# Optimization experiments

Hardware: AMD Instinct MI355X
Metric: run time of the kernel (lower is better)

The kernel has to match this reference:

```python
import jax, jax.numpy as jnp
import numpy as np

B, T_ENC, H, L, OUT, S_DEC = 32, 512, 512, 2, 128, 128
KV = 2 * H  # bidirectional encoder output width


def setup_inputs() -> dict:
    key = jax.random.key(0)
    ks = jax.random.split(key, 17)
    s = 0.05  # keep recurrent dynamics stable
    return {
        "encoder_output": jax.random.normal(ks[0], (B, T_ENC, KV), jnp.float32),
        "h0": jax.random.normal(ks[1], (L, B, H), jnp.float32) * s,
        "c0": jax.random.normal(ks[2], (L, B, H), jnp.float32) * s,
        "Wk": jax.random.normal(ks[3], (KV, KV), jnp.float32) * s,
        "Wq": jax.random.normal(ks[4], (KV, H), jnp.float32) * s,
        "Wv": jax.random.normal(ks[5], (KV, KV), jnp.float32) * s,
        "We": jax.random.normal(ks[6], (1, KV), jnp.float32) * s,
        "wih0": jax.random.normal(ks[7], (4 * H, OUT + KV), jnp.float32) * s,
        "whh0": jax.random.normal(ks[8], (4 * H, H), jnp.float32) * s,
        "bih0": jax.random.normal(ks[9], (4 * H,), jnp.float32) * s,
        "bhh0": jax.random.normal(ks[10], (4 * H,), jnp.float32) * s,
        "wih1": jax.random.normal(ks[11], (4 * H, H), jnp.float32) * s,
        "whh1": jax.random.normal(ks[12], (4 * H, H), jnp.float32) * s,
        "bih1": jax.random.normal(ks[13], (4 * H,), jnp.float32) * s,
        "bhh1": jax.random.normal(ks[14], (4 * H,), jnp.float32) * s,
        "fc_w": jax.random.normal(ks[15], (OUT, H), jnp.float32) * s,
        "fc_b": jax.random.normal(ks[16], (OUT,), jnp.float32) * s,
        "seq_length": S_DEC,
    }


def _lstm_cell(x, h, c, wih, whh, bih, bhh):
    # torch gate order: i, f, g, o
    g = x @ wih.T + h @ whh.T + bih + bhh
    i, f, gg, o = jnp.split(g, 4, axis=-1)
    c_new = jax.nn.sigmoid(f) * c + jax.nn.sigmoid(i) * jnp.tanh(gg)
    h_new = jax.nn.sigmoid(o) * jnp.tanh(c_new)
    return h_new, c_new


def reference(encoder_output, h0, c0, Wk, Wq, Wv, We, wih0, whh0, bih0, bhh0,
              wih1, whh1, bih1, bhh1, fc_w, fc_b, seq_length):
    # precomputed projections (key_layer / value_layer, no bias)
    key = encoder_output @ Wk.T      # [B, T_enc, KV]
    value = encoder_output @ Wv.T    # [B, T_enc, KV]

    def step(carry, _):
        h, c, y = carry  # h,c: [L,B,H]; y: [B,OUT]
        # Bahdanau attention, query = layer-0 hidden state
        q = h[0] @ Wq.T                                         # [B, KV]
        scores = jnp.einsum('btk,k->bt', jnp.tanh(q[:, None, :] + key), We[0])
        alpha = jax.nn.softmax(scores, axis=-1)                 # [B, T_enc]
        context = jnp.einsum('bt,btd->bd', alpha, value)        # [B, KV]
        x = jnp.concatenate([y, context], axis=-1)              # [B, OUT+KV]
        h0n, c0n = _lstm_cell(x, h[0], c[0], wih0, whh0, bih0, bhh0)
        h1n, c1n = _lstm_cell(h0n, h[1], c[1], wih1, whh1, bih1, bhh1)
        y_hat = jax.nn.relu(h1n @ fc_w.T + fc_b)                # [B, OUT]
        new_carry = (jnp.stack([h0n, h1n]), jnp.stack([c0n, c1n]), 1.0 + y_hat)
        return new_carry, y_hat

    y_init = jnp.zeros((h0.shape[1], fc_b.shape[0]), jnp.float32)  # SOS = 0.0
    _, ys = jax.lax.scan(step, (h0, c0, y_init), None, length=seq_length)
    return jnp.transpose(ys, (1, 0, 2))  # [B, seq_length, OUT]
```

## Files before the change

kernel.cpp:

```cpp
#include <hip/hip_runtime.h>
#include <hip/hip_bf16.h>
#include <cstdint>

#define TE    512
#define SD    128

typedef unsigned short u16;
typedef u16 u16x4 __attribute__((ext_vector_type(4)));
typedef u16 u16x8 __attribute__((ext_vector_type(8)));

#define QO    0
#define SCO   32768
#define CTXO  81920
#define YO    114688
#define H0O   118784
#define C0O   151552
#define H1O   184320
#define C1O   217088
#define ST_N  249856

__device__ __forceinline__ float b2f(u16 v) { return __uint_as_float(((unsigned)v) << 16); }
__device__ __forceinline__ u16 f2b(float f) {
  unsigned u = __float_as_uint(f);
  return (u16)((u + 0x7FFFu + ((u >> 16) & 1u)) >> 16);
}
__device__ __forceinline__ float tanh_f(float x) {
  float xc = fminf(12.f, fmaxf(-12.f, x));
  float e  = __expf(2.f * xc);
  return __fdividef(e - 1.f, e + 1.f);
}
__device__ __forceinline__ float sigm(float x) {
  float xc = fminf(30.f, fmaxf(-30.f, x));
  return __fdividef(1.f, 1.f + __expf(-xc));
}

__global__ __launch_bounds__(256)
void gemm_kv(const float* __restrict__ E, const float* __restrict__ Wk,
             const float* __restrict__ Wv, u16* __restrict__ key, u16* __restrict__ value) {
  const float* B = blockIdx.z ? Wv : Wk;
  u16* outp = blockIdx.z ? value : key;
  __shared__ float Asm[16][68], Bsm[16][68];
  const int tid = threadIdx.x;
  const int tm = blockIdx.x * 64, tn = blockIdx.y * 64;
  const int lr = tid >> 2, lc = (tid & 3) * 4;
  const int tx = tid & 15, ty = tid >> 4;
  float acc[4][4] = {};
  for (int k0 = 0; k0 < 1024; k0 += 16) {
    float4 av = *(const float4*)(&E[(long)(tm + lr) * 1024 + k0 + lc]);
    float4 bv = *(const float4*)(&B[(long)(tn + lr) * 1024 + k0 + lc]);
    Asm[lc][lr] = av.x; Asm[lc + 1][lr] = av.y; Asm[lc + 2][lr] = av.z; Asm[lc + 3][lr] = av.w;
    Bsm[lc][lr] = bv.x; Bsm[lc + 1][lr] = bv.y; Bsm[lc + 2][lr] = bv.z; Bsm[lc + 3][lr] = bv.w;
    __syncthreads();
#pragma unroll
    for (int kk = 0; kk < 16; ++kk) {
      float4 a4 = *(const float4*)(&Asm[kk][ty * 4]);
      float4 b4 = *(const float4*)(&Bsm[kk][tx * 4]);
      acc[0][0] += a4.x * b4.x; acc[0][1] += a4.x * b4.y; acc[0][2] += a4.x * b4.z; acc[0][3] += a4.x * b4.w;
      acc[1][0] += a4.y * b4.x; acc[1][1] += a4.y * b4.y; acc[1][2] += a4.y * b4.z; acc[1][3] += a4.y * b4.w;
      acc[2][0] += a4.z * b4.x; acc[2][1] += a4.z * b4.y; acc[2][2] += a4.z * b4.z; acc[2][3] += a4.z * b4.w;
      acc[3][0] += a4.w * b4.x; acc[3][1] += a4.w * b4.y; acc[3][2] += a4.w * b4.z; acc[3][3] += a4.w * b4.w;
    }
    __syncthreads();
  }
#pragma unroll
  for (int i = 0; i < 4; ++i)
#pragma unroll
    for (int j = 0; j < 4; ++j)
      outp[(long)(tm + ty * 4 + i) * 1024 + tn + tx * 4 + j] = f2b(acc[i][j]);
}

__global__ __launch_bounds__(256)
void init_state(const float* __restrict__ h0, const float* __restrict__ c0, float* __restrict__ st) {
  int i = blockIdx.x * 256 + threadIdx.x;
  st[H0O + i] = h0[i];
  st[H1O + i] = h0[16384 + i];
  st[C0O + i] = c0[i];
  st[C1O + i] = c0[16384 + i];
  if (i < 4096) st[YO + i] = 0.f;
}

__global__ __launch_bounds__(256)
void qproj(const float* __restrict__ h0, const float* __restrict__ Wq, float* __restrict__ st) {
  __shared__ float hr[512];
  const int b = blockIdx.x >> 2, o = (blockIdx.x & 3) * 256 + threadIdx.x;
  for (int i = threadIdx.x; i < 512; i += 256) hr[i] = h0[b * 512 + i];
  __syncthreads();
  float acc = 0.f;
  for (int k = 0; k < 512; k += 4) {
    float4 wv = *(const float4*)(&Wq[(long)o * 512 + k]);
    acc += hr[k] * wv.x + hr[k + 1] * wv.y + hr[k + 2] * wv.z + hr[k + 3] * wv.w;
  }
  st[QO + b * 1024 + o] = acc;
}

__global__ __launch_bounds__(256)
void stepA(const u16* __restrict__ key, const float* __restrict__ We, float* __restrict__ st) {
  const int tid = threadIdx.x, wv = tid >> 6, ln = tid & 63;
  const int b = blockIdx.x >> 4, tc = blockIdx.x & 15, t0 = tc * 32;
  float qr[16], wer[16];
  {
    const float* qp = st + QO + b * 1024 + ln * 16;
#pragma unroll
    for (int j = 0; j < 16; ++j) qr[j] = qp[j];
#pragma unroll
    for (int j = 0; j < 16; j += 4) {
      float4 w4 = *(const float4*)(&We[ln * 16 + j]);
      wer[j] = w4.x; wer[j + 1] = w4.y; wer[j + 2] = w4.z; wer[j + 3] = w4.w;
    }
  }
  const u16* kbase = key + ((long)(b * TE + t0) << 10) + ln * 16;
#pragma unroll
  for (int u = 0; u < 4; ++u) {
    const int tt0 = wv + u * 8, tt1 = wv + u * 8 + 4;
    const u16* kr0 = kbase + ((long)tt0 << 10);
    const u16* kr1 = kbase + ((long)tt1 << 10);
    u16x8 a0 = *(const u16x8*)kr0, a1 = *(const u16x8*)(kr0 + 8);
    u16x8 b0 = *(const u16x8*)kr1, b1 = *(const u16x8*)(kr1 + 8);
    float p0 = 0.f, p1 = 0.f;
#pragma unroll
    for (int j = 0; j < 8; ++j) {
      p0 += tanh_f(qr[j] + b2f(a0[j])) * wer[j];
      p1 += tanh_f(qr[j] + b2f(b0[j])) * wer[j];
    }
#pragma unroll
    for (int j = 0; j < 8; ++j) {
      p0 += tanh_f(qr[8 + j] + b2f(a1[j])) * wer[8 + j];
      p1 += tanh_f(qr[8 + j] + b2f(b1[j])) * wer[8 + j];
    }
    for (int off = 32; off; off >>= 1) {
      p0 += __shfl_down(p0, off);
      p1 += __shfl_down(p1, off);
    }
    if (ln == 0) {
      st[SCO + b * 512 + t0 + tt0] = p0;
      st[SCO + b * 512 + t0 + tt1] = p1;
    }
  }
}

__global__ __launch_bounds__(256)
void stepB(const u16* __restrict__ value, const float* __restrict__ fcw,
           const float* __restrict__ fcb, float* __restrict__ st,
           float* __restrict__ out, int s) {
  __shared__ float sm[1576];
  const int tid = threadIdx.x, wv = tid >> 6, ln = tid & 63;
  if (blockIdx.x < 256) {
    const int b = blockIdx.x >> 3, dc = blockIdx.x & 7;
    float* al = sm; float* rr = sm + 512; float* gp = sm + 520;
    al[tid]       = st[SCO + b * 512 + tid];
    al[tid + 256] = st[SCO + b * 512 + tid + 256];
    __syncthreads();
    float m = fmaxf(al[tid], al[tid + 256]);
    for (int off = 32; off; off >>= 1) m = fmaxf(m, __shfl_xor(m, off));
    if (ln == 0) rr[wv] = m;
    __syncthreads();
    const float M = fmaxf(fmaxf(rr[0], rr[1]), fmaxf(rr[2], rr[3]));
    float e0 = __expf(al[tid] - M), e1 = __expf(al[tid + 256] - M);
    float l = e0 + e1;
    for (int off = 32; off; off >>= 1) l += __shfl_xor(l, off);
    if (ln == 0) rr[4 + wv] = l;
    __syncthreads();
    const float inv = __fdividef(1.f, rr[4] + rr[5] + rr[6] + rr[7]);
    al[tid] = e0; al[tid + 256] = e1;
    __syncthreads();
    const int dl = (tid & 31) * 4, tg = tid >> 5;
    float a0 = 0.f, a1 = 0.f, a2 = 0.f, a3 = 0.f;
    const u16* vb = value + ((long)(b * TE) << 10) + dc * 128 + dl;
#pragma unroll 4
    for (int t = tg; t < 512; t += 8) {
      u16x4 vvv = *(const u16x4*)(vb + ((long)t << 10));
      float av = al[t];
      a0 += av * b2f(vvv[0]); a1 += av * b2f(vvv[1]);
      a2 += av * b2f(vvv[2]); a3 += av * b2f(vvv[3]);
    }
    float4 a4 = {a0, a1, a2, a3};
    *(float4*)(&gp[tg * 132 + dl]) = a4;
    __syncthreads();
    if (tid < 128) {
      float ssum = 0.f;
#pragma unroll
      for (int g = 0; g < 8; ++g) ssum += gp[g * 132 + tid];
      st[CTXO + b * 1024 + dc * 128 + tid] = ssum * inv;
    }
  } else if (s > 0) {
    float* h1s = sm;
    const int b = blockIdx.x - 256;
    const int p = s & 1;
    for (int i = tid; i < 512; i += 256) h1s[i] = st[H1O + p * 16384 + b * 512 + i];
    __syncthreads();
#pragma unroll
    for (int oi = 0; oi < 32; ++oi) {
      const int o = wv * 32 + oi;
      float part = 0.f;
#pragma unroll
      for (int kk = 0; kk < 8; ++kk) {
        int k = kk * 64 + ln;
        part += h1s[k] * fcw[(long)o * 512 + k];
      }
      for (int off = 32; off; off >>= 1) part += __shfl_down(part, off);
      if (ln == 0) {
        float yh = fmaxf(part + fcb[o], 0.f);
        out[((long)b * SD + (s - 1)) * 128 + o] = yh;
        st[YO + b * 128 + o] = 1.f + yh;
      }
    }
  }
}

__global__ __launch_bounds__(256)
void stepC(const float* __restrict__ wih0, const float* __restrict__ whh0,
           const float* __restrict__ bih0, const float* __restrict__ bhh0,
           float* __restrict__ st, int p) {
  __shared__ float xs[32 * 132];
  __shared__ float wr[8 * 132];
  __shared__ float gp[4 * 32 * 8];
  const int tid = threadIdx.x, wv = tid >> 6, ln = tid & 63;
  const int h0d = blockIdx.x * 2;
  float acc[8];
#pragma unroll
  for (int r = 0; r < 8; ++r) acc[r] = 0.f;
  for (int ch = 0; ch < 13; ++ch) {
    const float* src; int stride, col0;
    if (ch == 0)      { src = st + YO;               stride = 128;  col0 = 0; }
    else if (ch <= 8) { src = st + CTXO;             stride = 1024; col0 = (ch - 1) * 128; }
    else              { src = st + H0O + p * 16384;  stride = 512;  col0 = (ch - 9) * 128; }
#pragma unroll
    for (int i = 0; i < 4; ++i) {
      int e4 = tid * 4 + i * 1024;
      int bs = e4 >> 7, j = e4 & 127;
      *(float4*)(&xs[bs * 132 + j]) = *(const float4*)(src + bs * stride + col0 + j);
    }
    {
      int e = tid * 4, r = e >> 7, j = e & 127;
      int g = r >> 1, hh = r & 1;
      const float* wsrc; long rb;
      if (ch <= 8) { wsrc = wih0; rb = (long)(g * 512 + h0d + hh) * 1152 + ch * 128; }
      else         { wsrc = whh0; rb = (long)(g * 512 + h0d + hh) * 512 + (ch - 9) * 128; }
      *(float4*)(&wr[r * 132 + j]) = *(const float4*)(&wsrc[rb + j]);
    }
    __syncthreads();
    const int b = tid & 31, j0 = (tid >> 5) * 16;
#pragma unroll
    for (int jj = 0; jj < 16; jj += 4) {
      const float4 xv = *(const float4*)(&xs[b * 132 + j0 + jj]);
#pragma unroll
      for (int r = 0; r < 8; ++r) {
        const float4 w4 = *(const float4*)(&wr[r * 132 + j0 + jj]);
        acc[r] += xv.x * w4.x + xv.y * w4.y + xv.z * w4.z + xv.w * w4.w;
      }
    }
    __syncthreads();
  }
#pragma unroll
  for (int r = 0; r < 8; ++r) acc[r] += __shfl_down(acc[r], 32);
  if (ln < 32) {
#pragma unroll
    for (int r = 0; r < 8; ++r) gp[(wv * 32 + ln) * 8 + r] = acc[r];
  }
  __syncthreads();
  if (tid < 64) {
    const int b = tid & 31, hh = tid >> 5, h = h0d + hh;
    float gg[4];
#pragma unroll
    for (int g = 0; g < 4; ++g) {
      int r = g * 2 + hh;
      gg[g] = gp[(0 * 32 + b) * 8 + r] + gp[(1 * 32 + b) * 8 + r] +
              gp[(2 * 32 + b) * 8 + r] + gp[(3 * 32 + b) * 8 + r] +
              bih0[g * 512 + h] + bhh0[g * 512 + h];
    }
    float ig = sigm(gg[0]), fg = sigm(gg[1]), gt = tanh_f(gg[2]), og = sigm(gg[3]);
    int si = b * 512 + h;
    float c  = st[C0O + p * 16384 + si];
    float cn = fg * c + ig * gt;
    float hn = og * tanh_f(cn);
    st[H0O + (p ^ 1) * 16384 + si] = hn;
    st[C0O + (p ^ 1) * 16384 + si] = cn;
  }
}

__global__ __launch_bounds__(256)
void stepD(const float* __restrict__ wih1, const float* __restrict__ whh1,
           const float* __restrict__ bih1, const float* __restrict__ bhh1,
           const float* __restrict__ Wq, float* __restrict__ st, int p) {
  __shared__ float xs[32 * 132];
  __shared__ float wr[12 * 132];
  __shared__ float gp[4 * 32 * 12];
  const int tid = threadIdx.x, wv = tid >> 6, ln = tid & 63;
  const int h0d = blockIdx.x * 2;
  float acc[12];
#pragma unroll
  for (int r = 0; r < 12; ++r) acc[r] = 0.f;
  for (int ch = 0; ch < 8; ++ch) {
    const float* src = (ch < 4) ? (st + H0O + (p ^ 1) * 16384) : (st + H1O + p * 16384);
    const int col0 = (ch & 3) * 128;
#pragma unroll
    for (int i = 0; i < 4; ++i) {
      int e4 = tid * 4 + i * 1024;
      int bs = e4 >> 7, j = e4 & 127;
      *(float4*)(&xs[bs * 132 + j]) = *(const float4*)(src + bs * 512 + col0 + j);
    }
    {
      int e = tid * 4, r = e >> 7, j = e & 127;
      int g = r >> 1, hh = r & 1;
      const float* wsrc = (ch < 4) ? wih1 : whh1;
      long rb = (long)(g * 512 + h0d + hh) * 512 + col0;
      *(float4*)(&wr[r * 132 + j]) = *(const float4*)(&wsrc[rb + j]);
      if (ch < 4 && tid < 128) {
        int rq = e >> 7, j2 = e & 127;
        long rqb = (long)(4 * blockIdx.x + rq) * 512 + col0;
        *(float4*)(&wr[(8 + rq) * 132 + j2]) = *(const float4*)(&Wq[rqb + j2]);
      }
    }
    __syncthreads();
    const int b = tid & 31, j0 = (tid >> 5) * 16;
#pragma unroll
    for (int jj = 0; jj < 16; jj += 4) {
      const float4 xv = *(const float4*)(&xs[b * 132 + j0 + jj]);
#pragma unroll
      for (int r = 0; r < 8; ++r) {
        const float4 w4 = *(const float4*)(&wr[r * 132 + j0 + jj]);
        acc[r] += xv.x * w4.x + xv.y * w4.y + xv.z * w4.z + xv.w * w4.w;
      }
      if (ch < 4) {
#pragma unroll
        for (int r = 8; r < 12; ++r) {
          const float4 w4 = *(const float4*)(&wr[r * 132 + j0 + jj]);
          acc[r] += xv.x * w4.x + xv.y * w4.y + xv.z * w4.z + xv.w * w4.w;
        }
      }
    }
    __syncthreads();
  }
#pragma unroll
  for (int r = 0; r < 12; ++r) acc[r] += __shfl_down(acc[r], 32);
  if (ln < 32) {
#pragma unroll
    for (int r = 0; r < 12; ++r) gp[(wv * 32 + ln) * 12 + r] = acc[r];
  }
  __syncthreads();
  if (tid < 64) {
    const int b = tid & 31, hh = tid >> 5, h = h0d + hh;
    float gg[4];
#pragma unroll
    for (int g = 0; g < 4; ++g) {
      int r = g * 2 + hh;
      gg[g] = gp[(0 * 32 + b) * 12 + r] + gp[(1 * 32 + b) * 12 + r] +
              gp[(2 * 32 + b) * 12 + r] + gp[(3 * 32 + b) * 12 + r] +
              bih1[g * 512 + h] + bhh1[g * 512 + h];
    }
    float ig = sigm(gg[0]), fg = sigm(gg[1]), gt = tanh_f(gg[2]), og = sigm(gg[3]);
    int si = b * 512 + h;
    float c  = st[C1O + p * 16384 + si];
    float cn = fg * c + ig * gt;
    float hn = og * tanh_f(cn);
    st[H1O + (p ^ 1) * 16384 + si] = hn;
    st[C1O + (p ^ 1) * 16384 + si] = cn;
    int r0 = 8 + 2 * hh;
    float q0 = gp[(0 * 32 + b) * 12 + r0]     + gp[(1 * 32 + b) * 12 + r0] +
               gp[(2 * 32 + b) * 12 + r0]     + gp[(3 * 32 + b) * 12 + r0];
    float q1 = gp[(0 * 32 + b) * 12 + r0 + 1] + gp[(1 * 32 + b) * 12 + r0 + 1] +
               gp[(2 * 32 + b) * 12 + r0 + 1] + gp[(3 * 32 + b) * 12 + r0 + 1];
    int o0 = 4 * blockIdx.x + 2 * hh;
    st[QO + b * 1024 + o0]     = q0;
    st[QO + b * 1024 + o0 + 1] = q1;
  }
}

__global__ __launch_bounds__(256)
void fcK(const float* __restrict__ fcw, const float* __restrict__ fcb,
         float* __restrict__ st, float* __restrict__ out) {
  __shared__ float h1s[512];
  const int b = blockIdx.x >> 2, og = (blockIdx.x & 3) * 32;
  const int tid = threadIdx.x, wv = tid >> 6, ln = tid & 63;
  for (int i = tid; i < 512; i += 256) h1s[i] = st[H1O + b * 512 + i];
  __syncthreads();
#pragma unroll
  for (int oi = 0; oi < 8; ++oi) {
    const int o = og + wv * 8 + oi;
    float part = 0.f;
#pragma unroll
    for (int kk = 0; kk < 8; ++kk) {
      int k = kk * 64 + ln;
      part += h1s[k] * fcw[(long)o * 512 + k];
    }
    for (int off = 32; off; off >>= 1) part += __shfl_down(part, off);
    if (ln == 0) {
      float yh = fmaxf(part + fcb[o], 0.f);
      out[((long)b * SD + (SD - 1)) * 128 + o] = yh;
    }
  }
}

extern "C" void kernel_launch(void* const* d_in, const int* in_sizes, int n_in,
                              void* d_out, int out_size, void* d_ws, size_t ws_size,
                              hipStream_t stream) {
  (void)in_sizes; (void)n_in; (void)out_size; (void)ws_size;
  float* out = (float*)d_out;

  const float* E    = (const float*)d_in[0];
  const float* h0   = (const float*)d_in[1];
  const float* c0   = (const float*)d_in[2];
  const float* Wk   = (const float*)d_in[3];
  const float* Wq   = (const float*)d_in[4];
  const float* Wv   = (const float*)d_in[5];
  const float* We   = (const float*)d_in[6];
  const float* wih0 = (const float*)d_in[7];
  const float* whh0 = (const float*)d_in[8];
  const float* bih0 = (const float*)d_in[9];
  const float* bhh0 = (const float*)d_in[10];
  const float* wih1 = (const float*)d_in[11];
  const float* whh1 = (const float*)d_in[12];
  const float* bih1 = (const float*)d_in[13];
  const float* bhh1 = (const float*)d_in[14];
  const float* fcw  = (const float*)d_in[15];
  const float* fcb  = (const float*)d_in[16];

  u16* key   = (u16*)d_ws;
  u16* value = key + 16777216;
  float* st  = (float*)d_ws + 16777216;

  gemm_kv<<<dim3(256, 16, 2), 256, 0, stream>>>(E, Wk, Wv, key, value);
  init_state<<<64, 256, 0, stream>>>(h0, c0, st);
  qproj<<<128, 256, 0, stream>>>(h0, Wq, st);

  for (int s = 0; s < SD; ++s) {
    int p = s & 1;
    stepA<<<512, 256, 0, stream>>>(key, We, st);
    stepB<<<288, 256, 0, stream>>>(value, fcw, fcb, st, out, s);
    stepC<<<256, 256, 0, stream>>>(wih0, whh0, bih0, bhh0, st, p);
    stepD<<<256, 256, 0, stream>>>(wih1, whh1, bih1, bhh1, Wq, st, p);
  }
  fcK<<<128, 256, 0, stream>>>(fcw, fcb, st, out);
}
```

Measured before the change: 12.08 ms.

## Fuse per-step decoder kernels into one persistent kernel with grid barriers

```diff
diff --git a/kernel.cpp b/kernel.cpp
--- a/kernel.cpp
+++ b/kernel.cpp
@@ -4,6 +4,7 @@
 
 #define TE    512
 #define SD    128
+#define NB    512
 
 typedef unsigned short u16;
 typedef u16 u16x4 __attribute__((ext_vector_type(4)));
@@ -11,6 +12,7 @@
 
 #define QO    0
 #define SCO   32768
+#define BARO  49152
 #define CTXO  81920
 #define YO    114688
 #define H0O   118784
@@ -77,6 +79,7 @@
   st[C0O + i] = c0[i];
   st[C1O + i] = c0[16384 + i];
   if (i < 4096) st[YO + i] = 0.f;
+  if (i < 256) ((int*)(st + BARO))[i] = 0;
 }
 
 __global__ __launch_bounds__(256)
@@ -93,290 +96,26 @@
   st[QO + b * 1024 + o] = acc;
 }
 
-__global__ __launch_bounds__(256)
-void stepA(const u16* __restrict__ key, const float* __restrict__ We, float* __restrict__ st) {
-  const int tid = threadIdx.x, wv = tid >> 6, ln = tid & 63;
-  const int b = blockIdx.x >> 4, tc = blockIdx.x & 15, t0 = tc * 32;
-  float qr[16], wer[16];
-  {
-    const float* qp = st + QO + b * 1024 + ln * 16;
-#pragma unroll
-    for (int j = 0; j < 16; ++j) qr[j] = qp[j];
-#pragma unroll
-    for (int j = 0; j < 16; j += 4) {
-      float4 w4 = *(const float4*)(&We[ln * 16 + j]);
-      wer[j] = w4.x; wer[j + 1] = w4.y; wer[j + 2] = w4.z; wer[j + 3] = w4.w;
-    }
-  }
-  const u16* kbase = key + ((long)(b * TE + t0) << 10) + ln * 16;
-#pragma unroll
-  for (int u = 0; u < 4; ++u) {
-    const int tt0 = wv + u * 8, tt1 = wv + u * 8 + 4;
-    const u16* kr0 = kbase + ((long)tt0 << 10);
-    const u16* kr1 = kbase + ((long)tt1 << 10);
-    u16x8 a0 = *(const u16x8*)kr0, a1 = *(const u16x8*)(kr0 + 8);
-    u16x8 b0 = *(const u16x8*)kr1, b1 = *(const u16x8*)(kr1 + 8);
-    float p0 = 0.f, p1 = 0.f;
-#pragma unroll
-    for (int j = 0; j < 8; ++j) {
-      p0 += tanh_f(qr[j] + b2f(a0[j])) * wer[j];
-      p1 += tanh_f(qr[j] + b2f(b0[j])) * wer[j];
-    }
-#pragma unroll
-    for (int j = 0; j < 8; ++j) {
-      p0 += tanh_f(qr[8 + j] + b2f(a1[j])) * wer[8 + j];
-      p1 += tanh_f(qr[8 + j] + b2f(b1[j])) * wer[8 + j];
-    }
-    for (int off = 32; off; off >>= 1) {
-      p0 += __shfl_down(p0, off);
-      p1 += __shfl_down(p1, off);
-    }
-    if (ln == 0) {
-      st[SCO + b * 512 + t0 + tt0] = p0;
-      st[SCO + b * 512 + t0 + tt1] = p1;
-    }
-  }
-}
-
-__global__ __launch_bounds__(256)
-void stepB(const u16* __restrict__ value, const float* __restrict__ fcw,
-           const float* __restrict__ fcb, float* __restrict__ st,
-           float* __restrict__ out, int s) {
-  __shared__ float sm[1576];
-  const int tid = threadIdx.x, wv = tid >> 6, ln = tid & 63;
-  if (blockIdx.x < 256) {
-    const int b = blockIdx.x >> 3, dc = blockIdx.x & 7;
-    float* al = sm; float* rr = sm + 512; float* gp = sm + 520;
-    al[tid]       = st[SCO + b * 512 + tid];
-    al[tid + 256] = st[SCO + b * 512 + tid + 256];
-    __syncthreads();
-    float m = fmaxf(al[tid], al[tid + 256]);
-    for (int off = 32; off; off >>= 1) m = fmaxf(m, __shfl_xor(m, off));
-    if (ln == 0) rr[wv] = m;
-    __syncthreads();
-    const float M = fmaxf(fmaxf(rr[0], rr[1]), fmaxf(rr[2], rr[3]));
-    float e0 = __expf(al[tid] - M), e1 = __expf(al[tid + 256] - M);
-    float l = e0 + e1;
-    for (int off = 32; off; off >>= 1) l += __shfl_xor(l, off);
-    if (ln == 0) rr[4 + wv] = l;
-    __syncthreads();
-    const float inv = __fdividef(1.f, rr[4] + rr[5] + rr[6] + rr[7]);
-    al[tid] = e0; al[tid + 256] = e1;
-    __syncthreads();
-    const int dl = (tid & 31) * 4, tg = tid >> 5;
-    float a0 = 0.f, a1 = 0.f, a2 = 0.f, a3 = 0.f;
-    const u16* vb = value + ((long)(b * TE) << 10) + dc * 128 + dl;
-#pragma unroll 4
-    for (int t = tg; t < 512; t += 8) {
-      u16x4 vvv = *(const u16x4*)(vb + ((long)t << 10));
-      float av = al[t];
-      a0 += av * b2f(vvv[0]); a1 += av * b2f(vvv[1]);
-      a2 += av * b2f(vvv[2]); a3 += av * b2f(vvv[3]);
-    }
-    float4 a4 = {a0, a1, a2, a3};
-    *(float4*)(&gp[tg * 132 + dl]) = a4;
-    __syncthreads();
-    if (tid < 128) {
-      float ssum = 0.f;
-#pragma unroll
-      for (int g = 0; g < 8; ++g) ssum += gp[g * 132 + tid];
-      st[CTXO + b * 1024 + dc * 128 + tid] = ssum * inv;
-    }
-  } else if (s > 0) {
-    float* h1s = sm;
-    const int b = blockIdx.x - 256;
-    const int p = s & 1;
-    for (int i = tid; i < 512; i += 256) h1s[i] = st[H1O + p * 16384 + b * 512 + i];
-    __syncthreads();
-#pragma unroll
-    for (int oi = 0; oi < 32; ++oi) {
-      const int o = wv * 32 + oi;
-      float part = 0.f;
-#pragma unroll
-      for (int kk = 0; kk < 8; ++kk) {
-        int k = kk * 64 + ln;
-        part += h1s[k] * fcw[(long)o * 512 + k];
-      }
-      for (int off = 32; off; off >>= 1) part += __shfl_down(part, off);
-      if (ln == 0) {
-        float yh = fmaxf(part + fcb[o], 0.f);
-        out[((long)b * SD + (s - 1)) * 128 + o] = yh;
-        st[YO + b * 128 + o] = 1.f + yh;
-      }
-    }
-  }
-}
-
-__global__ __launch_bounds__(256)
-void stepC(const float* __restrict__ wih0, const float* __restrict__ whh0,
-           const float* __restrict__ bih0, const float* __restrict__ bhh0,
-           float* __restrict__ st, int p) {
-  __shared__ float xs[32 * 132];
-  __shared__ float wr[8 * 132];
-  __shared__ float gp[4 * 32 * 8];
-  const int tid = threadIdx.x, wv = tid >> 6, ln = tid & 63;
-  const int h0d = blockIdx.x * 2;
-  float acc[8];
-#pragma unroll
-  for (int r = 0; r < 8; ++r) acc[r] = 0.f;
-  for (int ch = 0; ch < 13; ++ch) {
-    const float* src; int stride, col0;
-    if (ch == 0)      { src = st + YO;               stride = 128;  col0 = 0; }
-    else if (ch <= 8) { src = st + CTXO;             stride = 1024; col0 = (ch - 1) * 128; }
-    else              { src = st + H0O + p * 16384;  stride = 512;  col0 = (ch - 9) * 128; }
-#pragma unroll
-    for (int i = 0; i < 4; ++i) {
-      int e4 = tid * 4 + i * 1024;
-      int bs = e4 >> 7, j = e4 & 127;
-      *(float4*)(&xs[bs * 132 + j]) = *(const float4*)(src + bs * stride + col0 + j);
-    }
-    {
-      int e = tid * 4, r = e >> 7, j = e & 127;
-      int g = r >> 1, hh = r & 1;
-      const float* wsrc; long rb;
-      if (ch <= 8) { wsrc = wih0; rb = (long)(g * 512 + h0d + hh) * 1152 + ch * 128; }
-      else         { wsrc = whh0; rb = (long)(g * 512 + h0d + hh) * 512 + (ch - 9) * 128; }
-      *(float4*)(&wr[r * 132 + j]) = *(const float4*)(&wsrc[rb + j]);
-    }
-    __syncthreads();
-    const int b = tid & 31, j0 = (tid >> 5) * 16;
-#pragma unroll
-    for (int jj = 0; jj < 16; jj += 4) {
-      const float4 xv = *(const float4*)(&xs[b * 132 + j0 + jj]);
-#pragma unroll
-      for (int r = 0; r < 8; ++r) {
-        const float4 w4 = *(const float4*)(&wr[r * 132 + j0 + jj]);
-        acc[r] += xv.x * w4.x + xv.y * w4.y + xv.z * w4.z + xv.w * w4.w;
-      }
-    }
-    __syncthreads();
-  }
-#pragma unroll
-  for (int r = 0; r < 8; ++r) acc[r] += __shfl_down(acc[r], 32);
-  if (ln < 32) {
-#pragma unroll
-    for (int r = 0; r < 8; ++r) gp[(wv * 32 + ln) * 8 + r] = acc[r];
+__device__ __forceinline__ void gbar(int* bar, int target) {
+  __syncthreads();
+  if (threadIdx.x == 0) {
+    __builtin_amdgcn_fence(__ATOMIC_RELEASE, "agent");
+    __hip_atomic_fetch_add(bar, 1, __ATOMIC_RELAXED, __HIP_MEMORY_SCOPE_AGENT);
+    while (__hip_atomic_load(bar, __ATOMIC_RELAXED, __HIP_MEMORY_SCOPE_AGENT) < target)
+      __builtin_amdgcn_s_sleep(8);
+    __builtin_amdgcn_fence(__ATOMIC_ACQUIRE, "agent");
   }
   __syncthreads();
-  if (tid < 64) {
-    const int b = tid & 31, hh = tid >> 5, h = h0d + hh;
-    float gg[4];
-#pragma unroll
-    for (int g = 0; g < 4; ++g) {
-      int r = g * 2 + hh;
-      gg[g] = gp[(0 * 32 + b) * 8 + r] + gp[(1 * 32 + b) * 8 + r] +
-              gp[(2 * 32 + b) * 8 + r] + gp[(3 * 32 + b) * 8 + r] +
-              bih0[g * 512 + h] + bhh0[g * 512 + h];
-    }
-    float ig = sigm(gg[0]), fg = sigm(gg[1]), gt = tanh_f(gg[2]), og = sigm(gg[3]);
-    int si = b * 512 + h;
-    float c  = st[C0O + p * 16384 + si];
-    float cn = fg * c + ig * gt;
-    float hn = og * tanh_f(cn);
-    st[H0O + (p ^ 1) * 16384 + si] = hn;
-    st[C0O + (p ^ 1) * 16384 + si] = cn;
-  }
-}
-
-__global__ __launch_bounds__(256)
-void stepD(const float* __restrict__ wih1, const float* __restrict__ whh1,
-           const float* __restrict__ bih1, const float* __restrict__ bhh1,
-           const float* __restrict__ Wq, float* __restrict__ st, int p) {
-  __shared__ float xs[32 * 132];
-  __shared__ float wr[12 * 132];
-  __shared__ float gp[4 * 32 * 12];
-  const int tid = threadIdx.x, wv = tid >> 6, ln = tid & 63;
-  const int h0d = blockIdx.x * 2;
-  float acc[12];
-#pragma unroll
-  for (int r = 0; r < 12; ++r) acc[r] = 0.f;
-  for (int ch = 0; ch < 8; ++ch) {
-    const float* src = (ch < 4) ? (st + H0O + (p ^ 1) * 16384) : (st + H1O + p * 16384);
-    const int col0 = (ch & 3) * 128;
-#pragma unroll
-    for (int i = 0; i < 4; ++i) {
-      int e4 = tid * 4 + i * 1024;
-      int bs = e4 >> 7, j = e4 & 127;
-      *(float4*)(&xs[bs * 132 + j]) = *(const float4*)(src + bs * 512 + col0 + j);
-    }
-    {
-      int e = tid * 4, r = e >> 7, j = e & 127;
-      int g = r >> 1, hh = r & 1;
-      const float* wsrc = (ch < 4) ? wih1 : whh1;
-      long rb = (long)(g * 512 + h0d + hh) * 512 + col0;
-      *(float4*)(&wr[r * 132 + j]) = *(const float4*)(&wsrc[rb + j]);
-      if (ch < 4 && tid < 128) {
-        int rq = e >> 7, j2 = e & 127;
-        long rqb = (long)(4 * blockIdx.x + rq) * 512 + col0;
-        *(float4*)(&wr[(8 + rq) * 132 + j2]) = *(const float4*)(&Wq[rqb + j2]);
-      }
-    }
-    __syncthreads();
-    const int b = tid & 31, j0 = (tid >> 5) * 16;
-#pragma unroll
-    for (int jj = 0; jj < 16; jj += 4) {
-      const float4 xv = *(const float4*)(&xs[b * 132 + j0 + jj]);
-#pragma unroll
-      for (int r = 0; r < 8; ++r) {
-        const float4 w4 = *(const float4*)(&wr[r * 132 + j0 + jj]);
-        acc[r] += xv.x * w4.x + xv.y * w4.y + xv.z * w4.z + xv.w * w4.w;
-      }
-      if (ch < 4) {
-#pragma unroll
-        for (int r = 8; r < 12; ++r) {
-          const float4 w4 = *(const float4*)(&wr[r * 132 + j0 + jj]);
-          acc[r] += xv.x * w4.x + xv.y * w4.y + xv.z * w4.z + xv.w * w4.w;
-        }
-      }
-    }
-    __syncthreads();
-  }
-#pragma unroll
-  for (int r = 0; r < 12; ++r) acc[r] += __shfl_down(acc[r], 32);
-  if (ln < 32) {
-#pragma unroll
-    for (int r = 0; r < 12; ++r) gp[(wv * 32 + ln) * 12 + r] = acc[r];
-  }
+}
+
+__device__ void fc_do(const float* __restrict__ fcw, const float* __restrict__ fcb,
+                      float* __restrict__ st, float* __restrict__ out,
+                      int b, int srow, int hp, int tid, int wv, int ln, float* sm) {
+  float* h1s = sm;
+  for (int i = tid; i < 512; i += 256) h1s[i] = st[H1O + hp * 16384 + b * 512 + i];
   __syncthreads();
-  if (tid < 64) {
-    const int b = tid & 31, hh = tid >> 5, h = h0d + hh;
-    float gg[4];
-#pragma unroll
-    for (int g = 0; g < 4; ++g) {
-      int r = g * 2 + hh;
-      gg[g] = gp[(0 * 32 + b) * 12 + r] + gp[(1 * 32 + b) * 12 + r] +
-              gp[(2 * 32 + b) * 12 + r] + gp[(3 * 32 + b) * 12 + r] +
-              bih1[g * 512 + h] + bhh1[g * 512 + h];
-    }
-    float ig = sigm(gg[0]), fg = sigm(gg[1]), gt = tanh_f(gg[2]), og = sigm(gg[3]);
-    int si = b * 512 + h;
-    float c  = st[C1O + p * 16384 + si];
-    float cn = fg * c + ig * gt;
-    float hn = og * tanh_f(cn);
-    st[H1O + (p ^ 1) * 16384 + si] = hn;
-    st[C1O + (p ^ 1) * 16384 + si] = cn;
-    int r0 = 8 + 2 * hh;
-    float q0 = gp[(0 * 32 + b) * 12 + r0]     + gp[(1 * 32 + b) * 12 + r0] +
-               gp[(2 * 32 + b) * 12 + r0]     + gp[(3 * 32 + b) * 12 + r0];
-    float q1 = gp[(0 * 32 + b) * 12 + r0 + 1] + gp[(1 * 32 + b) * 12 + r0 + 1] +
-               gp[(2 * 32 + b) * 12 + r0 + 1] + gp[(3 * 32 + b) * 12 + r0 + 1];
-    int o0 = 4 * blockIdx.x + 2 * hh;
-    st[QO + b * 1024 + o0]     = q0;
-    st[QO + b * 1024 + o0 + 1] = q1;
-  }
-}
-
-__global__ __launch_bounds__(256)
-void fcK(const float* __restrict__ fcw, const float* __restrict__ fcb,
-         float* __restrict__ st, float* __restrict__ out) {
-  __shared__ float h1s[512];
-  const int b = blockIdx.x >> 2, og = (blockIdx.x & 3) * 32;
-  const int tid = threadIdx.x, wv = tid >> 6, ln = tid & 63;
-  for (int i = tid; i < 512; i += 256) h1s[i] = st[H1O + b * 512 + i];
-  __syncthreads();
-#pragma unroll
-  for (int oi = 0; oi < 8; ++oi) {
-    const int o = og + wv * 8 + oi;
+  for (int oi = 0; oi < 32; ++oi) {
+    const int o = wv * 32 + oi;
     float part = 0.f;
 #pragma unroll
     for (int kk = 0; kk < 8; ++kk) {
@@ -386,9 +125,257 @@
     for (int off = 32; off; off >>= 1) part += __shfl_down(part, off);
     if (ln == 0) {
       float yh = fmaxf(part + fcb[o], 0.f);
-      out[((long)b * SD + (SD - 1)) * 128 + o] = yh;
+      out[((long)b * SD + srow) * 128 + o] = yh;
+      st[YO + b * 128 + o] = 1.f + yh;
     }
   }
+  __syncthreads();
+}
+
+__global__ __launch_bounds__(256, 2)
+void decode_all(const u16* __restrict__ key, const u16* __restrict__ value,
+                const float* __restrict__ We, const float* __restrict__ Wq,
+                const float* __restrict__ wih0, const float* __restrict__ whh0,
+                const float* __restrict__ bih0, const float* __restrict__ bhh0,
+                const float* __restrict__ wih1, const float* __restrict__ whh1,
+                const float* __restrict__ bih1, const float* __restrict__ bhh1,
+                const float* __restrict__ fcw, const float* __restrict__ fcb,
+                float* __restrict__ st, float* __restrict__ out) {
+  __shared__ float sm[5792];
+  int* bar = (int*)(st + BARO);
+  const int bid = blockIdx.x, tid = threadIdx.x;
+  const int wv = tid >> 6, ln = tid & 63;
+  int bnum = 0;
+
+  for (int s = 0; s < SD; ++s) {
+    const int p = s & 1;
+
+    {
+      const int b = bid >> 4, tc = bid & 15, t0 = tc * 32;
+      float qr[16], wer[16];
+      const float* qp = st + QO + b * 1024 + ln * 16;
+#pragma unroll
+      for (int j = 0; j < 16; ++j) qr[j] = qp[j];
+#pragma unroll
+      for (int j = 0; j < 16; j += 4) {
+        float4 w4 = *(const float4*)(&We[ln * 16 + j]);
+        wer[j] = w4.x; wer[j + 1] = w4.y; wer[j + 2] = w4.z; wer[j + 3] = w4.w;
+      }
+      const u16* kbase = key + ((long)(b * TE + t0) << 10) + ln * 16;
+#pragma unroll
+      for (int u = 0; u < 4; ++u) {
+        const int tt0 = wv + u * 8, tt1 = wv + u * 8 + 4;
+        const u16* kr0 = kbase + ((long)tt0 << 10);
+        const u16* kr1 = kbase + ((long)tt1 << 10);
+        u16x8 a0 = *(const u16x8*)kr0, a1 = *(const u16x8*)(kr0 + 8);
+        u16x8 b0 = *(const u16x8*)kr1, b1 = *(const u16x8*)(kr1 + 8);
+        float p0 = 0.f, p1 = 0.f;
+#pragma unroll
+        for (int j = 0; j < 8; ++j) {
+          p0 += tanh_f(qr[j] + b2f(a0[j])) * wer[j];
+          p1 += tanh_f(qr[j] + b2f(b0[j])) * wer[j];
+        }
+#pragma unroll
+        for (int j = 0; j < 8; ++j) {
+          p0 += tanh_f(qr[8 + j] + b2f(a1[j])) * wer[8 + j];
+          p1 += tanh_f(qr[8 + j] + b2f(b1[j])) * wer[8 + j];
+        }
+        for (int off = 32; off; off >>= 1) {
+          p0 += __shfl_down(p0, off);
+          p1 += __shfl_down(p1, off);
+        }
+        if (ln == 0) {
+          st[SCO + b * 512 + t0 + tt0] = p0;
+          st[SCO + b * 512 + t0 + tt1] = p1;
+        }
+      }
+    }
+    gbar(bar, (++bnum) * NB);
+
+    if (bid < 256) {
+      const int b = bid >> 3, dc = bid & 7;
+      float* al = sm; float* rr = sm + 512; float* gp = sm + 520;
+      al[tid]       = st[SCO + b * 512 + tid];
+      al[tid + 256] = st[SCO + b * 512 + tid + 256];
+      __syncthreads();
+      float m = fmaxf(al[tid], al[tid + 256]);
+      for (int off = 32; off; off >>= 1) m = fmaxf(m, __shfl_xor(m, off));
+      if (ln == 0) rr[wv] = m;
+      __syncthreads();
+      const float M = fmaxf(fmaxf(rr[0], rr[1]), fmaxf(rr[2], rr[3]));
+      float e0 = __expf(al[tid] - M), e1 = __expf(al[tid + 256] - M);
+      float l = e0 + e1;
+      for (int off = 32; off; off >>= 1) l += __shfl_xor(l, off);
+      if (ln == 0) rr[4 + wv] = l;
+      __syncthreads();
+      const float inv = __fdividef(1.f, rr[4] + rr[5] + rr[6] + rr[7]);
+      al[tid] = e0; al[tid + 256] = e1;
+      __syncthreads();
+      const int dl = (tid & 31) * 4, tg = tid >> 5;
+      float a0 = 0.f, a1 = 0.f, a2 = 0.f, a3 = 0.f;
+      const u16* vb = value + ((long)(b * TE) << 10) + dc * 128 + dl;
+#pragma unroll 4
+      for (int t = tg; t < 512; t += 8) {
+        u16x4 vvv = *(const u16x4*)(vb + ((long)t << 10));
+        float av = al[t];
+        a0 += av * b2f(vvv[0]); a1 += av * b2f(vvv[1]);
+        a2 += av * b2f(vvv[2]); a3 += av * b2f(vvv[3]);
+      }
+      float4 a4 = {a0, a1, a2, a3};
+      *(float4*)(&gp[tg * 132 + dl]) = a4;
+      __syncthreads();
+      if (tid < 128) {
+        float ssum = 0.f;
+#pragma unroll
+        for (int g = 0; g < 8; ++g) ssum += gp[g * 132 + tid];
+        st[CTXO + b * 1024 + dc * 128 + tid] = ssum * inv;
+      }
+    } else if (bid < 288) {
+      if (s > 0) fc_do(fcw, fcb, st, out, bid - 256, s - 1, p, tid, wv, ln, sm);
+    }
+    gbar(bar, (++bnum) * NB);
+
+    {
+      const int h = bid;
+      float* xs = sm; float* wr = sm + 4224; float* gp = sm + 4752;
+      float acc[4] = {0.f, 0.f, 0.f, 0.f};
+      for (int ch = 0; ch < 13; ++ch) {
+        const float* src; int stride, col0;
+        if (ch == 0)      { src = st + YO;               stride = 128;  col0 = 0; }
+        else if (ch <= 8) { src = st + CTXO;             stride = 1024; col0 = (ch - 1) * 128; }
+        else              { src = st + H0O + p * 16384;  stride = 512;  col0 = (ch - 9) * 128; }
+#pragma unroll
+        for (int i = 0; i < 4; ++i) {
+          int e4 = tid * 4 + i * 1024;
+          int bs = e4 >> 7, j = e4 & 127;
+          *(float4*)(&xs[bs * 132 + j]) = *(const float4*)(src + bs * stride + col0 + j);
+        }
+        {
+          int e = tid * 2, r = e >> 7, j = e & 127;
+          const float* wsrc; long rb;
+          if (ch <= 8) { wsrc = wih0; rb = (long)(r * 512 + h) * 1152 + ch * 128; }
+          else         { wsrc = whh0; rb = (long)(r * 512 + h) * 512 + (ch - 9) * 128; }
+          *(float2*)(&wr[r * 132 + j]) = *(const float2*)(&wsrc[rb + j]);
+        }
+        __syncthreads();
+        const int b = tid & 31, j0 = (tid >> 5) * 16;
+#pragma unroll
+        for (int jj = 0; jj < 16; jj += 4) {
+          const float4 xv = *(const float4*)(&xs[b * 132 + j0 + jj]);
+#pragma unroll
+          for (int r = 0; r < 4; ++r) {
+            const float4 w4 = *(const float4*)(&wr[r * 132 + j0 + jj]);
+            acc[r] += xv.x * w4.x + xv.y * w4.y + xv.z * w4.z + xv.w * w4.w;
+          }
+        }
+        __syncthreads();
+      }
+#pragma unroll
+      for (int r = 0; r < 4; ++r) acc[r] += __shfl_down(acc[r], 32);
+      if (ln < 32) {
+#pragma unroll
+        for (int r = 0; r < 4; ++r) gp[(wv * 32 + ln) * 4 + r] = acc[r];
+      }
+      __syncthreads();
+      if (tid < 32) {
+        const int b = tid;
+        float gg[4];
+#pragma unroll
+        for (int g = 0; g < 4; ++g)
+          gg[g] = gp[(0 * 32 + b) * 4 + g] + gp[(1 * 32 + b) * 4 + g] +
+                  gp[(2 * 32 + b) * 4 + g] + gp[(3 * 32 + b) * 4 + g] +
+                  bih0[g * 512 + h] + bhh0[g * 512 + h];
+        float ig = sigm(gg[0]), fg = sigm(gg[1]), gt = tanh_f(gg[2]), og = sigm(gg[3]);
+        int si = b * 512 + h;
+        float c  = st[C0O + p * 16384 + si];
+        float cn = fg * c + ig * gt;
+        float hn = og * tanh_f(cn);
+        st[H0O + (p ^ 1) * 16384 + si] = hn;
+        st[C0O + (p ^ 1) * 16384 + si] = cn;
+      }
+      __syncthreads();
+    }
+    gbar(bar, (++bnum) * NB);
+
+    {
+      const int h = bid;
+      float* xs = sm; float* wr = sm + 4224; float* gp = sm + 5016;
+      float acc[6] = {0.f, 0.f, 0.f, 0.f, 0.f, 0.f};
+      for (int ch = 0; ch < 8; ++ch) {
+        const float* src = (ch < 4) ? (st + H0O + (p ^ 1) * 16384) : (st + H1O + p * 16384);
+        const int col0 = (ch & 3) * 128;
+#pragma unroll
+        for (int i = 0; i < 4; ++i) {
+          int e4 = tid * 4 + i * 1024;
+          int bs = e4 >> 7, j = e4 & 127;
+          *(float4*)(&xs[bs * 132 + j]) = *(const float4*)(src + bs * 512 + col0 + j);
+        }
+        {
+          int e = tid * 2, r = e >> 7, j = e & 127;
+          const float* wsrc = (ch < 4) ? wih1 : whh1;
+          long rb = (long)(r * 512 + h) * 512 + col0;
+          *(float2*)(&wr[r * 132 + j]) = *(const float2*)(&wsrc[rb + j]);
+          if (ch < 4) {
+            int rq = tid >> 7, j2 = tid & 127;
+            wr[(4 + rq) * 132 + j2] = Wq[(long)(2 * h + rq) * 512 + col0 + j2];
+          }
+        }
+        __syncthreads();
+        const int b = tid & 31, j0 = (tid >> 5) * 16;
+#pragma unroll
+        for (int jj = 0; jj < 16; jj += 4) {
+          const float4 xv = *(const float4*)(&xs[b * 132 + j0 + jj]);
+#pragma unroll
+          for (int r = 0; r < 4; ++r) {
+            const float4 w4 = *(const float4*)(&wr[r * 132 + j0 + jj]);
+            acc[r] += xv.x * w4.x + xv.y * w4.y + xv.z * w4.z + xv.w * w4.w;
+          }
+          if (ch < 4) {
+#pragma unroll
+            for (int r = 4; r < 6; ++r) {
+              const float4 w4 = *(const float4*)(&wr[r * 132 + j0 + jj]);
+              acc[r] += xv.x * w4.x + xv.y * w4.y + xv.z * w4.z + xv.w * w4.w;
+            }
+          }
+        }
+        __syncthreads();
+      }
+#pragma unroll
+      for (int r = 0; r < 6; ++r) acc[r] += __shfl_down(acc[r], 32);
+      if (ln < 32) {
+#pragma unroll
+        for (int r = 0; r < 6; ++r) gp[(wv * 32 + ln) * 6 + r] = acc[r];
+      }
+      __syncthreads();
+      if (tid < 32) {
+        const int b = tid;
+        float gg[4];
+#pragma unroll
+        for (int g = 0; g < 4; ++g)
+          gg[g] = gp[(0 * 32 + b) * 6 + g] + gp[(1 * 32 + b) * 6 + g] +
+                  gp[(2 * 32 + b) * 6 + g] + gp[(3 * 32 + b) * 6 + g] +
+                  bih1[g * 512 + h] + bhh1[g * 512 + h];
+        float ig = sigm(gg[0]), fg = sigm(gg[1]), gt = tanh_f(gg[2]), og = sigm(gg[3]);
+        int si = b * 512 + h;
+        float c  = st[C1O + p * 16384 + si];
+        float cn = fg * c + ig * gt;
+        float hn = og * tanh_f(cn);
+        st[H1O + (p ^ 1) * 16384 + si] = hn;
+        st[C1O + (p ^ 1) * 16384 + si] = cn;
+        float q0 = gp[(0 * 32 + b) * 6 + 4] + gp[(1 * 32 + b) * 6 + 4] +
+                   gp[(2 * 32 + b) * 6 + 4] + gp[(3 * 32 + b) * 6 + 4];
+        float q1 = gp[(0 * 32 + b) * 6 + 5] + gp[(1 * 32 + b) * 6 + 5] +
+                   gp[(2 * 32 + b) * 6 + 5] + gp[(3 * 32 + b) * 6 + 5];
+        st[QO + b * 1024 + 2 * h]     = q0;
+        st[QO + b * 1024 + 2 * h + 1] = q1;
+      }
+      __syncthreads();
+    }
+    gbar(bar, (++bnum) * NB);
+  }
+
+  if (bid >= 256 && bid < 288)
+    fc_do(fcw, fcb, st, out, bid - 256, SD - 1, 0, tid, wv, ln, sm);
 }
 
 extern "C" void kernel_launch(void* const* d_in, const int* in_sizes, int n_in,
@@ -422,13 +409,6 @@
   gemm_kv<<<dim3(256, 16, 2), 256, 0, stream>>>(E, Wk, Wv, key, value);
   init_state<<<64, 256, 0, stream>>>(h0, c0, st);
   qproj<<<128, 256, 0, stream>>>(h0, Wq, st);
-
-  for (int s = 0; s < SD; ++s) {
-    int p = s & 1;
-    stepA<<<512, 256, 0, stream>>>(key, We, st);
-    stepB<<<288, 256, 0, stream>>>(value, fcw, fcb, st, out, s);
-    stepC<<<256, 256, 0, stream>>>(wih0, whh0, bih0, bhh0, st, p);
-    stepD<<<256, 256, 0, stream>>>(wih1, whh1, bih1, bhh1, Wq, st, p);
-  }
-  fcK<<<128, 256, 0, stream>>>(fcw, fcb, st, out);
-}
+  decode_all<<<NB, 256, 0, stream>>>(key, value, We, Wq, wih0, whh0, bih0, bhh0,
+                                     wih1, whh1, bih1, bhh1, fcw, fcb, st, out);
+}
```

After: 35.17 ms. 2.91x slower.
